# Performance work log

Measured on AMD Instinct MI355X. Metric: run time of the kernel, lower is better.

## Reference

```python
import jax, jax.numpy as jnp
import numpy as np

K_NEIGHBORS = 16  # n_sample

# Each Conv1x1+BatchNorm (eval mode) stage is an exact per-channel affine map,
# so it is represented by a single fused (W, b) pair: y = W @ x + b.

def affine(W, b, x):
    # W: [Cout, Cin]; x: [B, Cin, N] or [B, Cin, N, K]
    if x.ndim == 3:
        return jnp.einsum('oc,bcn->bon', W, x) + b[None, :, None]
    return jnp.einsum('oc,bcnk->bonk', W, x) + b[None, :, None, None]

def knn_idx(p, k):
    # p: [B, N, 3] -> idx of k nearest neighbors (incl. self): [B, N, k]
    sq = jnp.sum(p * p, axis=-1)  # [B, N]
    d2 = sq[:, :, None] + sq[:, None, :] - 2.0 * jnp.einsum('bnc,bmc->bnm', p, p)
    _, idx = jax.lax.top_k(-d2, k)
    return idx

def group(feat, idx):
    # feat: [B, C, N], idx: [B, N, K] -> grouped[b,c,n,k] = feat[b,c,idx[b,n,k]]
    return jax.vmap(lambda f, i: f[:, i])(feat, idx)


def setup_inputs() -> dict:
    key = jax.random.key(0)
    B, C, N = 4, 128, 4096
    ks = jax.random.split(key, 22)
    def w(k, o, i):
        return (jax.random.normal(k, (o, i), jnp.float32) / np.sqrt(i)).astype(jnp.float32)
    def bv(k, o):
        return (jax.random.normal(k, (o,), jnp.float32) * 0.01).astype(jnp.float32)
    inp = {
        'input_p': jax.random.normal(ks[0], (B, 3, N), jnp.float32),
        'input_x': jax.random.normal(ks[1], (B, C, N), jnp.float32),
        'top_W': w(ks[2], C, C),   'top_b': bv(ks[3], C),
        'down_W': w(ks[4], C, C),  'down_b': bv(ks[5], C),
        'phi_W': w(ks[6], C, C),   'phi_b': bv(ks[7], C),
        'psi_W': w(ks[8], C, C),   'psi_b': bv(ks[9], C),
        'alpha_W': w(ks[10], C, C), 'alpha_b': bv(ks[11], C),
        'g1_W': w(ks[12], C, C),   'g1_b': bv(ks[13], C),
        'g2_W': w(ks[14], C, C),   'g2_b': bv(ks[15], C),
        'd1_W': w(ks[16], C, 3),   'd1_b': bv(ks[17], C),
        'd2_W': w(ks[18], C, C),   'd2_b': bv(ks[19], C),
        'a': 0, 'b': 0,
    }
    return inp


def reference(input_p, input_x, top_W, top_b, down_W, down_b, phi_W, phi_b,
              psi_W, psi_b, alpha_W, alpha_b, g1_W, g1_b, g2_W, g2_b,
              d1_W, d1_b, d2_W, d2_b, a, b):
    res = input_x
    p = jnp.transpose(input_p, (0, 2, 1))          # [B, N, 3]
    idx = knn_idx(p, K_NEIGHBORS)                  # [B, N, K]
    grouped_p = group(input_p, idx)                # [B, 3, N, K]
    x = affine(top_W, top_b, input_x)              # linear_top
    phi = affine(phi_W, phi_b, x)[:, :, :, None]   # [B, C, N, 1] (broadcast over K)
    psi = group(affine(psi_W, psi_b, x), idx)      # [B, C, N, K]
    alp = group(affine(alpha_W, alpha_b, x), idx)  # [B, C, N, K]
    rel = input_p[:, :, :, None] - grouped_p       # relative xyz [B, 3, N, K]
    pos = affine(d2_W, d2_b, jax.nn.relu(affine(d1_W, d1_b, rel)))   # delta MLP
    attn = affine(g2_W, g2_b, jax.nn.relu(affine(g1_W, g1_b, phi - psi + pos)))  # gamma MLP
    y = (jax.nn.softmax(attn, axis=-1) * (alp + pos)).sum(axis=-1)   # [B, C, N]
    y = affine(down_W, down_b, y)                  # linear_down
    return y + res
```

## Files before the change

kernel.cpp:

```cpp
#include <hip/hip_runtime.h>
#include <hip/hip_bf16.h>

#define BB 4
#define CC 128
#define NN 4096
#define KK 16
#define FLT_BIG 3.402823466e+38f

typedef __attribute__((ext_vector_type(8))) short short8v;
typedef __attribute__((ext_vector_type(4))) short short4v;
typedef __attribute__((ext_vector_type(4))) float f32x4;

__device__ __forceinline__ unsigned short f2b(float x) {
  union { float f; unsigned u; } v; v.f = x;
  unsigned r = v.u + 0x7fffu + ((v.u >> 16) & 1u);
  return (unsigned short)(r >> 16);
}
__device__ __forceinline__ float b2f(unsigned short h) {
  union { float f; unsigned u; } v; v.u = ((unsigned)h) << 16; return v.f;
}
__device__ __forceinline__ unsigned pkrn(float a, float b) {
  __hip_bfloat162 t = __float22bfloat162_rn(make_float2(a, b));
  union { __hip_bfloat162 h; unsigned u; } c; c.h = t; return c.u;
}
__device__ __forceinline__ void split2(float a, float b, unsigned& h, unsigned& l) {
  h = pkrn(a, b);
  union { unsigned u; float f; } lo, hi2;
  lo.u = h << 16;
  hi2.u = h & 0xffff0000u;
  l = pkrn(a - lo.f, b - hi2.f);
}

__device__ __forceinline__ float dist4(const float4 q, const float4 c) {
  float t = __fmaf_rn(q.x, c.x, __fmaf_rn(q.y, c.y, __fmul_rn(q.z, c.z)));
  return __fmaf_rn(-2.f, t, q.w + c.w);
}

__global__ __launch_bounds__(256) void setup_kernel(
    const float* __restrict__ p, const float* __restrict__ x,
    const float* __restrict__ d2W, const float* __restrict__ g1W,
    const float* __restrict__ g2W, const float* __restrict__ topW,
    const float* __restrict__ phiW, const float* __restrict__ psiW,
    const float* __restrict__ alpW, const float* __restrict__ dnW,
    float4* __restrict__ pkg, unsigned short* __restrict__ wpk,
    unsigned short* __restrict__ xh, unsigned short* __restrict__ xl)
{
  __shared__ float t[64][65];
  const int bid = blockIdx.x, tid = threadIdx.x;
  if (bid < 64) {
    int i = bid * 256 + tid;
    int b = i >> 12, m = i & (NN - 1);
    const float* pb = p + (size_t)b * 3 * NN;
    float xx = pb[m], yy = pb[NN + m], zz = pb[2 * NN + m];
    pkg[i] = make_float4(xx, yy, zz, __fmaf_rn(xx, xx, __fmaf_rn(yy, yy, __fmul_rn(zz, zz))));
  } else if (bid < 128) {
    int tt = (bid - 64) * 256 + tid;
    int mat = tt >> 11, r = tt & 2047;
    int ct = r >> 8, ks = (r >> 6) & 3, lane = r & 63;
    const float* W;
    switch (mat) {
      case 0: W = d2W; break;  case 1: W = g1W; break;
      case 2: W = g2W; break;  case 3: W = topW; break;
      case 4: W = phiW; break; case 5: W = psiW; break;
      case 6: W = alpW; break; default: W = dnW; break;
    }
    int row = ct * 16 + (lane & 15);
    int k0 = ks * 32 + (lane >> 4) * 8;
    const float* src = &W[row * 128 + k0];
    unsigned short* dh = &wpk[((size_t)(((mat * 2 + 0) * 8 + ct) * 4 + ks) * 64 + lane) * 8];
    unsigned short* dl = &wpk[((size_t)(((mat * 2 + 1) * 8 + ct) * 4 + ks) * 64 + lane) * 8];
#pragma unroll
    for (int e = 0; e < 8; ++e) {
      float v = src[e];
      unsigned short h = f2b(v);
      dh[e] = h;
      dl[e] = f2b(v - b2f(h));
    }
  } else {
    int bid2 = bid - 128;
    int nb = bid2 & 63, cb = (bid2 >> 6) & 1, b = bid2 >> 7;
    const int c0 = cb * 64, n0 = nb * 64;
    const int tn = tid & 63, tq = tid >> 6;
    const float* xb = x + ((size_t)b * CC + c0) * NN + n0;
#pragma unroll
    for (int i = 0; i < 16; ++i) {
      int c = tq * 16 + i;
      t[c][tn] = xb[(size_t)c * NN + tn];
    }
    __syncthreads();
#pragma unroll
    for (int i = 0; i < 16; ++i) {
      int nl = tq * 16 + i;
      float v = t[tn][nl];
      unsigned short h = f2b(v);
      size_t o = ((size_t)b * NN + n0 + nl) * CC + c0 + tn;
      xh[o] = h;
      xl[o] = f2b(v - b2f(h));
    }
  }
}

__global__ __launch_bounds__(512, 2) void knn_kernel(const float4* __restrict__ pkg,
                                                     int* __restrict__ outidx)
{
  __shared__ float BD[8][64][17];
  __shared__ float4 CH[8][64];
  __shared__ float TS[64];
  __shared__ int   CNT[64];
  __shared__ float COLd[64][20];
  __shared__ int   COLi[64][20];
  const int b = blockIdx.y;
  const int tid = threadIdx.x;
  const int lane = tid & 63;
  const int w = tid >> 6;
  const int n = blockIdx.x * 64 + lane;
  const float4* PB = pkg + (size_t)b * NN;
  const float4 qc = PB[n];
  if (tid < 64) CNT[tid] = 0;

  float bd[16];
#pragma unroll
  for (int t = 0; t < 16; ++t) bd[t] = FLT_BIG;
  const int m0 = w * 512;

  {
    float4 nxt = PB[m0 + lane];
    for (int c = 0; c < 8; ++c) {
      CH[w][lane] = nxt;
      if (c < 7) nxt = PB[m0 + (c + 1) * 64 + lane];
#pragma unroll 4
      for (int e = 0; e < 64; ++e) {
        float4 cd = CH[w][e];
        float d = dist4(qc, cd);
#pragma unroll
        for (int t = 15; t >= 1; --t) bd[t] = __builtin_amdgcn_fmed3f(bd[t - 1], d, bd[t]);
        bd[0] = fminf(bd[0], d);
      }
    }
  }
#pragma unroll
  for (int t = 0; t < 16; ++t) BD[w][lane][t] = bd[t];
  __syncthreads();

  if (tid < 64) {
    const int q = tid;
    int h0 = 0, h1 = 0, h2 = 0, h3 = 0, h4 = 0, h5 = 0, h6 = 0, h7 = 0;
    float mv = FLT_BIG;
#pragma unroll 1
    for (int r = 0; r < 16; ++r) {
      float v0 = BD[0][q][h0], v1 = BD[1][q][h1], v2 = BD[2][q][h2], v3 = BD[3][q][h3];
      float v4 = BD[4][q][h4], v5 = BD[5][q][h5], v6 = BD[6][q][h6], v7 = BD[7][q][h7];
      mv = v0; int mw = 0;
      if (v1 < mv) { mv = v1; mw = 1; }
      if (v2 < mv) { mv = v2; mw = 2; }
      if (v3 < mv) { mv = v3; mw = 3; }
      if (v4 < mv) { mv = v4; mw = 4; }
      if (v5 < mv) { mv = v5; mw = 5; }
      if (v6 < mv) { mv = v6; mw = 6; }
      if (v7 < mv) { mv = v7; mw = 7; }
      h0 += (mw == 0); h1 += (mw == 1); h2 += (mw == 2); h3 += (mw == 3);
      h4 += (mw == 4); h5 += (mw == 5); h6 += (mw == 6); h7 += (mw == 7);
    }
    TS[q] = mv;
  }
  __syncthreads();

  {
    const float thr = TS[lane];
    float4 nxt = PB[m0 + lane];
    for (int c = 0; c < 8; ++c) {
      CH[w][lane] = nxt;
      if (c < 7) nxt = PB[m0 + (c + 1) * 64 + lane];
#pragma unroll 4
      for (int e = 0; e < 64; ++e) {
        float4 cd = CH[w][e];
        float d = dist4(qc, cd);
        if (d <= thr) {
          int pos = atomicAdd(&CNT[lane], 1);
          if (pos < 20) { COLd[lane][pos] = d; COLi[lane][pos] = m0 + c * 64 + e; }
        }
      }
    }
  }
  __syncthreads();

  if (tid < 64) {
    const int q = tid;
    int c = CNT[q]; if (c > 20) c = 20;
    int* op = outidx + ((size_t)b * NN + blockIdx.x * 64 + q) * KK;
    if (c == KK) {
#pragma unroll
      for (int o = 0; o < KK; ++o) op[o] = COLi[q][o];
    } else {
      const float T = TS[q];
      int less = 0;
      for (int s = 0; s < c; ++s) less += (COLd[q][s] < T);
      int need = KK - less;
      int o = 0;
      for (int s = 0; s < c; ++s)
        if (COLd[q][s] < T) op[o++] = COLi[q][s];
      for (int s = 0; s < c; ++s) {
        if (COLd[q][s] == T) {
          int idx = COLi[q][s];
          int rank = 0;
          for (int s2 = 0; s2 < c; ++s2)
            rank += (COLd[q][s2] == T && COLi[q][s2] < idx);
          if (rank < need) op[o++] = idx;
        }
      }
    }
  }
}

__global__ __launch_bounds__(256) void feat_kernel(
    const unsigned short* __restrict__ xh, const unsigned short* __restrict__ xl,
    const unsigned short* __restrict__ wpk,
    const float* __restrict__ topb, const float* __restrict__ phib,
    const float* __restrict__ psib, const float* __restrict__ alpb,
    float* __restrict__ phit, float* __restrict__ psit,
    unsigned short* __restrict__ alpt)
{
  __shared__ float xtile[32][129];
  const int b = blockIdx.y, n0 = blockIdx.x * 32;
  const int tid = threadIdx.x, l = tid & 63, w = tid >> 6;
  const int lr = l & 15, lh = l >> 4;
  const int nt = w & 1, cq = w >> 1;
  {
    const int nrow = n0 + nt * 16 + lr;
    const unsigned short* xhp = xh + ((size_t)b * NN + nrow) * CC;
    const unsigned short* xlp = xl + ((size_t)b * NN + nrow) * CC;
    short8v Ah[4], Al[4];
#pragma unroll
    for (int ks = 0; ks < 4; ++ks) {
      Ah[ks] = *(const short8v*)&xhp[ks * 32 + lh * 8];
      Al[ks] = *(const short8v*)&xlp[ks * 32 + lh * 8];
    }
    const int nDl = nt * 16 + lh * 4;
#pragma unroll
    for (int cc = 0; cc < 4; ++cc) {
      const int colt = cq * 4 + cc;
      f32x4 acc = (f32x4){0.f, 0.f, 0.f, 0.f};
#pragma unroll
      for (int ks = 0; ks < 4; ++ks) {
        short8v Wh = *(const short8v*)&wpk[((size_t)(((3 * 2 + 0) * 8 + colt) * 4 + ks) * 64 + l) * 8];
        short8v Wl = *(const short8v*)&wpk[((size_t)(((3 * 2 + 1) * 8 + colt) * 4 + ks) * 64 + l) * 8];
        acc = __builtin_amdgcn_mfma_f32_16x16x32_bf16(Ah[ks], Wh, acc, 0, 0, 0);
        acc = __builtin_amdgcn_mfma_f32_16x16x32_bf16(Al[ks], Wh, acc, 0, 0, 0);
        acc = __builtin_amdgcn_mfma_f32_16x16x32_bf16(Ah[ks], Wl, acc, 0, 0, 0);
      }
      float bv = topb[colt * 16 + lr];
#pragma unroll
      for (int r = 0; r < 4; ++r) xtile[nDl + r][colt * 16 + lr] = acc[r] + bv;
    }
  }
  __syncthreads();
  short8v Ah[4], Al[4];
  {
    const int rl = nt * 16 + lr;
#pragma unroll
    for (int ks = 0; ks < 4; ++ks) {
      union { short8v s; unsigned u[4]; } H, L;
#pragma unroll
      for (int i = 0; i < 4; ++i) {
        float a = xtile[rl][ks * 32 + lh * 8 + 2 * i];
        float bb = xtile[rl][ks * 32 + lh * 8 + 2 * i + 1];
        split2(a, bb, H.u[i], L.u[i]);
      }
      Ah[ks] = H.s; Al[ks] = L.s;
    }
  }
  const int nD = n0 + nt * 16 + lh * 4;
#pragma unroll
  for (int m = 0; m < 3; ++m) {
    const int mat = 4 + m;
    const float* bias = (m == 0) ? phib : (m == 1) ? psib : alpb;
#pragma unroll
    for (int cc = 0; cc < 4; ++cc) {
      const int colt = cq * 4 + cc;
      f32x4 acc = (f32x4){0.f, 0.f, 0.f, 0.f};
#pragma unroll
      for (int ks = 0; ks < 4; ++ks) {
        short8v Wh = *(const short8v*)&wpk[((size_t)(((mat * 2 + 0) * 8 + colt) * 4 + ks) * 64 + l) * 8];
        short8v Wl = *(const short8v*)&wpk[((size_t)(((mat * 2 + 1) * 8 + colt) * 4 + ks) * 64 + l) * 8];
        acc = __builtin_amdgcn_mfma_f32_16x16x32_bf16(Ah[ks], Wh, acc, 0, 0, 0);
        acc = __builtin_amdgcn_mfma_f32_16x16x32_bf16(Al[ks], Wh, acc, 0, 0, 0);
        acc = __builtin_amdgcn_mfma_f32_16x16x32_bf16(Ah[ks], Wl, acc, 0, 0, 0);
      }
      float bv = bias[colt * 16 + lr];
      if (m == 2) {
#pragma unroll
        for (int r = 0; r < 4; ++r)
          alpt[((size_t)b * NN + nD + r) * CC + colt * 16 + lr] = f2b(acc[r] + bv);
      } else {
        float* outp = (m == 0) ? phit : psit;
#pragma unroll
        for (int r = 0; r < 4; ++r)
          outp[((size_t)b * NN + nD + r) * CC + colt * 16 + lr] = acc[r] + bv;
      }
    }
  }
}

__global__ __launch_bounds__(256) void down_kernel(
    const unsigned short* __restrict__ yh, const unsigned short* __restrict__ yl,
    const unsigned short* __restrict__ wpk,
    const float* __restrict__ bias, const float* __restrict__ res,
    float* __restrict__ out)
{
  const int b = blockIdx.y, n0 = blockIdx.x * 64;
  const int tid = threadIdx.x, l = tid & 63, w = tid >> 6;
  const int lr = l & 15, lh = l >> 4;
  short8v Ah[2][4], Al[2][4];
#pragma unroll
  for (int ct = 0; ct < 2; ++ct)
#pragma unroll
    for (int ks = 0; ks < 4; ++ks) {
      Ah[ct][ks] = *(const short8v*)&wpk[((size_t)(((7 * 2 + 0) * 8 + (2 * w + ct)) * 4 + ks) * 64 + l) * 8];
      Al[ct][ks] = *(const short8v*)&wpk[((size_t)(((7 * 2 + 1) * 8 + (2 * w + ct)) * 4 + ks) * 64 + l) * 8];
    }
  f32x4 acc[2][4];
#pragma unroll
  for (int colt = 0; colt < 4; ++colt) {
    const int n = n0 + colt * 16 + lr;
    const unsigned short* yhp = yh + ((size_t)b * NN + n) * CC;
    const unsigned short* ylp = yl + ((size_t)b * NN + n) * CC;
#pragma unroll
    for (int ct = 0; ct < 2; ++ct) acc[ct][colt] = (f32x4){0.f, 0.f, 0.f, 0.f};
#pragma unroll
    for (int ks = 0; ks < 4; ++ks) {
      short8v Bh = *(const short8v*)&yhp[ks * 32 + lh * 8];
      short8v Bl = *(const short8v*)&ylp[ks * 32 + lh * 8];
#pragma unroll
      for (int ct = 0; ct < 2; ++ct) {
        acc[ct][colt] = __builtin_amdgcn_mfma_f32_16x16x32_bf16(Ah[ct][ks], Bh, acc[ct][colt], 0, 0, 0);
        acc[ct][colt] = __builtin_amdgcn_mfma_f32_16x16x32_bf16(Ah[ct][ks], Bl, acc[ct][colt], 0, 0, 0);
        acc[ct][colt] = __builtin_amdgcn_mfma_f32_16x16x32_bf16(Al[ct][ks], Bh, acc[ct][colt], 0, 0, 0);
      }
    }
  }
#pragma unroll
  for (int ct = 0; ct < 2; ++ct) {
    const int c0 = 32 * w + ct * 16 + lh * 4;
#pragma unroll
    for (int r = 0; r < 4; ++r) {
      float bv = bias[c0 + r];
#pragma unroll
      for (int colt = 0; colt < 4; ++colt) {
        size_t o = ((size_t)b * CC + c0 + r) * NN + n0 + colt * 16 + lr;
        out[o] = acc[ct][colt][r] + bv + res[o];
      }
    }
  }
}

#define TNP 4
#define ASW(row, c) ((c) ^ (((row) & 7) << 3))
__global__ __launch_bounds__(256, 4) void fused_kernel(
    const float* __restrict__ p, const int* __restrict__ idxg,
    const float* __restrict__ phi_t, const float* __restrict__ psi_t,
    const unsigned short* __restrict__ alp_b, const unsigned short* __restrict__ wpk,
    const float* __restrict__ d1W, const float* __restrict__ d1b,
    const float* __restrict__ d2b, const float* __restrict__ g1b,
    const float* __restrict__ g2b,
    unsigned short* __restrict__ yh, unsigned short* __restrict__ yl)
{
  __shared__ __align__(16) unsigned short act[2][64][136];
  __shared__ int idxs[64];
  const int b = blockIdx.y;
  const int n0 = blockIdx.x * TNP;
  const int tid = threadIdx.x;
  const int l = tid & 63, w = tid >> 6;
  const int lr = l & 15, lh = l >> 4;

  if (tid < 64) idxs[tid] = idxg[((size_t)b * NN + n0 + (tid >> 4)) * KK + (tid & 15)];
  __syncthreads();

  {
    const int col = tid & 63, q = tid >> 6;
    const int pt = col >> 4;
    const int j = idxs[col];
    const float* pb = p + (size_t)b * 3 * NN;
    float r0 = pb[n0 + pt] - pb[j];
    float r1 = pb[NN + n0 + pt] - pb[NN + j];
    float r2 = pb[2 * NN + n0 + pt] - pb[2 * NN + j];
#pragma unroll
    for (int ch = 0; ch < 4; ++ch) {
      int c0 = q * 32 + ch * 8;
      float v[8];
#pragma unroll
      for (int e = 0; e < 8; ++e) {
        int c = c0 + e;
        v[e] = fmaxf(d1W[c * 3 + 0] * r0 + d1W[c * 3 + 1] * r1 + d1W[c * 3 + 2] * r2 + d1b[c], 0.f);
      }
      uint4 H, L;
      split2(v[0], v[1], H.x, L.x); split2(v[2], v[3], H.y, L.y);
      split2(v[4], v[5], H.z, L.z); split2(v[6], v[7], H.w, L.w);
      *(uint4*)&act[0][col][ASW(col, c0)] = H;
      *(uint4*)&act[1][col][ASW(col, c0)] = L;
    }
  }
  __syncthreads();

  int idxv[TNP];
#pragma unroll
  for (int colt = 0; colt < TNP; ++colt) idxv[colt] = idxs[colt * 16 + lr];

  f32x4 acc[2][TNP];
  short8v Af[2][4];

#define LOADA(MAT) do {                                                                 \
  _Pragma("unroll") for (int ct = 0; ct < 2; ++ct)                                      \
    _Pragma("unroll") for (int ks = 0; ks < 4; ++ks)                                    \
      Af[ct][ks] = *(const short8v*)&wpk[((size_t)((((MAT) * 2 + 0) * 8 + (2 * w + ct)) * 4 + ks) * 64 + l) * 8]; \
  } while (0)

#define MMUL() do {                                                                     \
  _Pragma("unroll") for (int ct = 0; ct < 2; ++ct)                                      \
    _Pragma("unroll") for (int colt = 0; colt < TNP; ++colt)                            \
      acc[ct][colt] = (f32x4){0.f, 0.f, 0.f, 0.f};                                      \
  _Pragma("unroll") for (int colt = 0; colt < TNP; ++colt) {                            \
    const int row_ = colt * 16 + lr;                                                    \
    short8v Bh[4], Bl[4];                                                               \
    _Pragma("unroll") for (int ks = 0; ks < 4; ++ks) {                                  \
      Bh[ks] = *(const short8v*)&act[0][row_][ASW(row_, ks * 32 + lh * 8)];             \
      Bl[ks] = *(const short8v*)&act[1][row_][ASW(row_, ks * 32 + lh * 8)];             \
    }                                                                                   \
    _Pragma("unroll") for (int ct = 0; ct < 2; ++ct)                                    \
      _Pragma("unroll") for (int ks = 0; ks < 4; ++ks) {                                \
        acc[ct][colt] = __builtin_amdgcn_mfma_f32_16x16x32_bf16(Af[ct][ks], Bh[ks],     \
                                                                acc[ct][colt], 0, 0, 0); \
        acc[ct][colt] = __builtin_amdgcn_mfma_f32_16x16x32_bf16(Af[ct][ks], Bl[ks],     \
                                                                acc[ct][colt], 0, 0, 0); \
      }                                                                                 \
  } } while (0)

  LOADA(0); MMUL();
  float pos[2][TNP][4];
#pragma unroll
  for (int ct = 0; ct < 2; ++ct) {
    f32x4 bv = *(const f32x4*)&d2b[32 * w + ct * 16 + lh * 4];
#pragma unroll
    for (int colt = 0; colt < TNP; ++colt)
#pragma unroll
      for (int r = 0; r < 4; ++r) pos[ct][colt][r] = acc[ct][colt][r] + bv[r];
  }
  __syncthreads();

#pragma unroll
  for (int colt = 0; colt < TNP; ++colt) {
    size_t prow = ((size_t)b * NN + n0 + colt) * CC;
    size_t srow = ((size_t)b * NN + idxv[colt]) * CC;
#pragma unroll
    for (int ct = 0; ct < 2; ++ct) {
      int c0 = 32 * w + ct * 16 + lh * 4;
      f32x4 ph = *(const f32x4*)&phi_t[prow + c0];
      f32x4 ps = *(const f32x4*)&psi_t[srow + c0];
      float v[4];
#pragma unroll
      for (int r = 0; r < 4; ++r) v[r] = pos[ct][colt][r] + ph[r] - ps[r];
      uint2 H, L;
      split2(v[0], v[1], H.x, L.x); split2(v[2], v[3], H.y, L.y);
      const int row = colt * 16 + lr;
      *(uint2*)&act[0][row][ASW(row, c0)] = H;
      *(uint2*)&act[1][row][ASW(row, c0)] = L;
    }
  }
  __syncthreads();

  LOADA(1); MMUL();
  __syncthreads();
#pragma unroll
  for (int ct = 0; ct < 2; ++ct) {
    f32x4 bv = *(const f32x4*)&g1b[32 * w + ct * 16 + lh * 4];
    int c0 = 32 * w + ct * 16 + lh * 4;
#pragma unroll
    for (int colt = 0; colt < TNP; ++colt) {
      float v[4];
#pragma unroll
      for (int r = 0; r < 4; ++r) v[r] = fmaxf(acc[ct][colt][r] + bv[r], 0.f);
      uint2 H, L;
      split2(v[0], v[1], H.x, L.x); split2(v[2], v[3], H.y, L.y);
      const int row = colt * 16 + lr;
      *(uint2*)&act[0][row][ASW(row, c0)] = H;
      *(uint2*)&act[1][row][ASW(row, c0)] = L;
    }
  }
  __syncthreads();

  LOADA(2); MMUL();
#pragma unroll
  for (int ct = 0; ct < 2; ++ct) {
    f32x4 bv = *(const f32x4*)&g2b[32 * w + ct * 16 + lh * 4];
#pragma unroll
    for (int colt = 0; colt < TNP; ++colt)
#pragma unroll
      for (int r = 0; r < 4; ++r) acc[ct][colt][r] += bv[r];
  }

#pragma unroll
  for (int ct = 0; ct < 2; ++ct)
#pragma unroll
    for (int colt = 0; colt < TNP; ++colt)
#pragma unroll
      for (int r = 0; r < 4; ++r) {
        float a = acc[ct][colt][r];
        float m = __shfl(a, l & 48);
        float e = __expf(a - m);
        float s = e;
        s += __shfl_xor(s, 1);
        s += __shfl_xor(s, 2);
        s += __shfl_xor(s, 4);
        s += __shfl_xor(s, 8);
        acc[ct][colt][r] = e * __builtin_amdgcn_rcpf(s);
      }

  __syncthreads();
  unsigned short* yst = &act[0][0][0];

#pragma unroll
  for (int colt = 0; colt < TNP; ++colt) {
    size_t arow = ((size_t)b * NN + idxv[colt]) * CC;
#pragma unroll
    for (int ct = 0; ct < 2; ++ct) {
      int c0 = 32 * w + ct * 16 + lh * 4;
      uint2 ua = *(const uint2*)&alp_b[arow + c0];
      union { unsigned u; float f; } a0, a1, a2, a3;
      a0.u = ua.x << 16; a1.u = ua.x & 0xffff0000u;
      a2.u = ua.y << 16; a3.u = ua.y & 0xffff0000u;
      float av[4] = {a0.f, a1.f, a2.f, a3.f};
      float yv[4];
#pragma unroll
      for (int r = 0; r < 4; ++r) {
        float part = acc[ct][colt][r] * (av[r] + pos[ct][colt][r]);
        part += __shfl_xor(part, 1);
        part += __shfl_xor(part, 2);
        part += __shfl_xor(part, 4);
        part += __shfl_xor(part, 8);
        yv[r] = part;
      }
      if (lr == 0) {
        uint2 H, L;
        split2(yv[0], yv[1], H.x, L.x); split2(yv[2], yv[3], H.y, L.y);
        *(uint2*)&yst[(size_t)colt * 128 + c0] = H;
        *(uint2*)&yst[(size_t)(4 + colt) * 128 + c0] = L;
      }
    }
  }
  __syncthreads();
  if (tid < 128) {
    int plane = tid >> 6, row = (tid >> 4) & 3, chunk = tid & 15;
    uint4 v4 = *(const uint4*)&yst[(size_t)(plane * 4 + row) * 128 + chunk * 8];
    unsigned short* dst = (plane ? yl : yh) + ((size_t)b * NN + n0 + row) * CC + chunk * 8;
    *(uint4*)dst = v4;
  }
#undef LOADA
#undef MMUL
}

extern "C" void kernel_launch(void* const* d_in, const int* in_sizes, int n_in,
                              void* d_out, int out_size, void* d_ws, size_t ws_size,
                              hipStream_t stream) {
  const float* input_p = (const float*)d_in[0];
  const float* input_x = (const float*)d_in[1];
  const float* top_W   = (const float*)d_in[2];  const float* top_b   = (const float*)d_in[3];
  const float* down_W  = (const float*)d_in[4];  const float* down_b  = (const float*)d_in[5];
  const float* phi_W   = (const float*)d_in[6];  const float* phi_b   = (const float*)d_in[7];
  const float* psi_W   = (const float*)d_in[8];  const float* psi_b   = (const float*)d_in[9];
  const float* alpha_W = (const float*)d_in[10]; const float* alpha_b = (const float*)d_in[11];
  const float* g1_W    = (const float*)d_in[12]; const float* g1_b    = (const float*)d_in[13];
  const float* g2_W    = (const float*)d_in[14]; const float* g2_b    = (const float*)d_in[15];
  const float* d1_W    = (const float*)d_in[16]; const float* d1_b    = (const float*)d_in[17];
  const float* d2_W    = (const float*)d_in[18]; const float* d2_b    = (const float*)d_in[19];
  float* out = (float*)d_out;

  char* ws = (char*)d_ws;
  int*            ws_idx   = (int*)ws;
  unsigned short* ws_xin_h = (unsigned short*)(ws + (size_t)1  * (1 << 20));
  unsigned short* ws_xin_l = (unsigned short*)(ws + (size_t)5  * (1 << 20));
  float*          ws_phi   = (float*)(ws + (size_t)9  * (1 << 20));
  float*          ws_psi   = (float*)(ws + (size_t)17 * (1 << 20));
  unsigned short* ws_alp   = (unsigned short*)(ws + (size_t)25 * (1 << 20));
  float4*         ws_pkg   = (float4*)(ws + (size_t)29 * (1 << 20));
  unsigned short* ws_wpk   = (unsigned short*)(ws + (size_t)29 * (1 << 20) + (1 << 18));
  unsigned short* ws_y_h = ws_xin_h;
  unsigned short* ws_y_l = ws_xin_l;

  setup_kernel<<<640, 256, 0, stream>>>(input_p, input_x, d2_W, g1_W, g2_W, top_W,
                                        phi_W, psi_W, alpha_W, down_W,
                                        ws_pkg, ws_wpk, ws_xin_h, ws_xin_l);
  knn_kernel<<<dim3(NN / 64, BB), 512, 0, stream>>>(ws_pkg, ws_idx);
  feat_kernel<<<dim3(NN / 32, BB), 256, 0, stream>>>(ws_xin_h, ws_xin_l, ws_wpk,
                                                     top_b, phi_b, psi_b, alpha_b,
                                                     ws_phi, ws_psi, ws_alp);
  fused_kernel<<<dim3(NN / TNP, BB), 256, 0, stream>>>(input_p, ws_idx, ws_phi, ws_psi, ws_alp,
                                                       ws_wpk, d1_W, d1_b, d2_b, g1_b, g2_b,
                                                       ws_y_h, ws_y_l);
  down_kernel<<<dim3(NN / 64, BB), 256, 0, stream>>>(ws_y_h, ws_y_l, ws_wpk, down_b,
                                                     input_x, out);
}
```

Before: 368.9 us.

## Store psi as bf16 and drop LDS XOR swizzle in fused kernel

The psi feature tensor is now written by feat_kernel as bf16 instead of fp32 and is unpacked to float in fused_kernel, which halves the bytes of the gathered psi reads. The workspace layout is compacted to match. Separately, the XOR swizzle on the activation LDS tiles is removed and plain padded indexing (row stride 136) is used, relying on the padding to avoid bank conflicts. Psi precision drops to bf16, which could affect accuracy of the attention logits.

```diff
diff --git a/kernel.cpp b/kernel.cpp
--- a/kernel.cpp
+++ b/kernel.cpp
@@ -217,7 +217,7 @@
     const unsigned short* __restrict__ wpk,
     const float* __restrict__ topb, const float* __restrict__ phib,
     const float* __restrict__ psib, const float* __restrict__ alpb,
-    float* __restrict__ phit, float* __restrict__ psit,
+    float* __restrict__ phit, unsigned short* __restrict__ psit,
     unsigned short* __restrict__ alpt)
 {
   __shared__ float xtile[32][129];
@@ -287,15 +287,15 @@
         acc = __builtin_amdgcn_mfma_f32_16x16x32_bf16(Ah[ks], Wl, acc, 0, 0, 0);
       }
       float bv = bias[colt * 16 + lr];
-      if (m == 2) {
+      if (m == 0) {
 #pragma unroll
         for (int r = 0; r < 4; ++r)
-          alpt[((size_t)b * NN + nD + r) * CC + colt * 16 + lr] = f2b(acc[r] + bv);
+          phit[((size_t)b * NN + nD + r) * CC + colt * 16 + lr] = acc[r] + bv;
       } else {
-        float* outp = (m == 0) ? phit : psit;
+        unsigned short* outp = (m == 1) ? psit : alpt;
 #pragma unroll
         for (int r = 0; r < 4; ++r)
-          outp[((size_t)b * NN + nD + r) * CC + colt * 16 + lr] = acc[r] + bv;
+          outp[((size_t)b * NN + nD + r) * CC + colt * 16 + lr] = f2b(acc[r] + bv);
       }
     }
   }
@@ -354,10 +354,9 @@
 }
 
 #define TNP 4
-#define ASW(row, c) ((c) ^ (((row) & 7) << 3))
 __global__ __launch_bounds__(256, 4) void fused_kernel(
     const float* __restrict__ p, const int* __restrict__ idxg,
-    const float* __restrict__ phi_t, const float* __restrict__ psi_t,
+    const float* __restrict__ phi_t, const unsigned short* __restrict__ psi_b,
     const unsigned short* __restrict__ alp_b, const unsigned short* __restrict__ wpk,
     const float* __restrict__ d1W, const float* __restrict__ d1b,
     const float* __restrict__ d2b, const float* __restrict__ g1b,
@@ -395,8 +394,8 @@
       uint4 H, L;
       split2(v[0], v[1], H.x, L.x); split2(v[2], v[3], H.y, L.y);
       split2(v[4], v[5], H.z, L.z); split2(v[6], v[7], H.w, L.w);
-      *(uint4*)&act[0][col][ASW(col, c0)] = H;
-      *(uint4*)&act[1][col][ASW(col, c0)] = L;
+      *(uint4*)&act[0][col][c0] = H;
+      *(uint4*)&act[1][col][c0] = L;
     }
   }
   __syncthreads();
@@ -422,8 +421,8 @@
     const int row_ = colt * 16 + lr;                                                    \
     short8v Bh[4], Bl[4];                                                               \
     _Pragma("unroll") for (int ks = 0; ks < 4; ++ks) {                                  \
-      Bh[ks] = *(const short8v*)&act[0][row_][ASW(row_, ks * 32 + lh * 8)];             \
-      Bl[ks] = *(const short8v*)&act[1][row_][ASW(row_, ks * 32 + lh * 8)];             \
+      Bh[ks] = *(const short8v*)&act[0][row_][ks * 32 + lh * 8];                        \
+      Bl[ks] = *(const short8v*)&act[1][row_][ks * 32 + lh * 8];                        \
     }                                                                                   \
     _Pragma("unroll") for (int ct = 0; ct < 2; ++ct)                                    \
       _Pragma("unroll") for (int ks = 0; ks < 4; ++ks) {                                \
@@ -454,15 +453,19 @@
     for (int ct = 0; ct < 2; ++ct) {
       int c0 = 32 * w + ct * 16 + lh * 4;
       f32x4 ph = *(const f32x4*)&phi_t[prow + c0];
-      f32x4 ps = *(const f32x4*)&psi_t[srow + c0];
+      uint2 up = *(const uint2*)&psi_b[srow + c0];
+      union { unsigned u; float f; } p0, p1, p2, p3;
+      p0.u = up.x << 16; p1.u = up.x & 0xffff0000u;
+      p2.u = up.y << 16; p3.u = up.y & 0xffff0000u;
+      float psv[4] = {p0.f, p1.f, p2.f, p3.f};
       float v[4];
 #pragma unroll
-      for (int r = 0; r < 4; ++r) v[r] = pos[ct][colt][r] + ph[r] - ps[r];
+      for (int r = 0; r < 4; ++r) v[r] = pos[ct][colt][r] + ph[r] - psv[r];
       uint2 H, L;
       split2(v[0], v[1], H.x, L.x); split2(v[2], v[3], H.y, L.y);
       const int row = colt * 16 + lr;
-      *(uint2*)&act[0][row][ASW(row, c0)] = H;
-      *(uint2*)&act[1][row][ASW(row, c0)] = L;
+      *(uint2*)&act[0][row][c0] = H;
+      *(uint2*)&act[1][row][c0] = L;
     }
   }
   __syncthreads();
@@ -481,8 +484,8 @@
       uint2 H, L;
       split2(v[0], v[1], H.x, L.x); split2(v[2], v[3], H.y, L.y);
       const int row = colt * 16 + lr;
-      *(uint2*)&act[0][row][ASW(row, c0)] = H;
-      *(uint2*)&act[1][row][ASW(row, c0)] = L;
+      *(uint2*)&act[0][row][c0] = H;
+      *(uint2*)&act[1][row][c0] = L;
     }
   }
   __syncthreads();
@@ -578,10 +581,10 @@
   unsigned short* ws_xin_h = (unsigned short*)(ws + (size_t)1  * (1 << 20));
   unsigned short* ws_xin_l = (unsigned short*)(ws + (size_t)5  * (1 << 20));
   float*          ws_phi   = (float*)(ws + (size_t)9  * (1 << 20));
-  float*          ws_psi   = (float*)(ws + (size_t)17 * (1 << 20));
-  unsigned short* ws_alp   = (unsigned short*)(ws + (size_t)25 * (1 << 20));
-  float4*         ws_pkg   = (float4*)(ws + (size_t)29 * (1 << 20));
-  unsigned short* ws_wpk   = (unsigned short*)(ws + (size_t)29 * (1 << 20) + (1 << 18));
+  unsigned short* ws_psi   = (unsigned short*)(ws + (size_t)17 * (1 << 20));
+  unsigned short* ws_alp   = (unsigned short*)(ws + (size_t)21 * (1 << 20));
+  float4*         ws_pkg   = (float4*)(ws + (size_t)25 * (1 << 20));
+  unsigned short* ws_wpk   = (unsigned short*)(ws + (size_t)25 * (1 << 20) + (1 << 18));
   unsigned short* ws_y_h = ws_xin_h;
   unsigned short* ws_y_l = ws_xin_l;
 
```

Measured after the change: 322.1 us. -12.7%, faster.
